# Optimization experiments

Hardware: AMD Instinct MI355X
Metric: run time of the kernel (lower is better)

The kernel has to match this reference:

```python
import jax, jax.numpy as jnp
import numpy as np

DIM = 256
HEADS = 8
WIN = 8
N = WIN * WIN          # 64 tokens per window
NW = 1024              # windows per image (256x256 map, 8x8 windows)
BATCH = 4
B_ = BATCH * NW        # 4096
HEAD_DIM = DIM // HEADS


def _relative_position_index():
    # identical to the torch buffer construction in WindowAttention.__init__
    coords = np.stack(np.meshgrid(np.arange(WIN), np.arange(WIN), indexing='ij'))  # [2,W,W]
    flat = coords.reshape(2, -1)                                # [2, N]
    rel = flat[:, :, None] - flat[:, None, :]                   # [2, N, N]
    rel = rel.transpose(1, 2, 0).copy()                         # [N, N, 2]
    rel[:, :, 0] += WIN - 1
    rel[:, :, 1] += WIN - 1
    rel[:, :, 0] *= 2 * WIN - 1
    return jnp.asarray(rel.sum(-1), dtype=jnp.int32)            # [N, N], values in [0, 225)


def setup_inputs() -> dict:
    key = jax.random.key(0)
    ks = jax.random.split(key, 9)
    std = 0.02
    return {
        'x': jax.random.normal(ks[0], (B_, N, DIM), dtype=jnp.float32),
        'mask': jax.random.normal(ks[1], (NW, N, N), dtype=jnp.float32),
        'w_q': jax.random.normal(ks[2], (DIM, DIM), dtype=jnp.float32) * std,
        'b_q': jnp.zeros((DIM,), dtype=jnp.float32),
        'w_kv': jax.random.normal(ks[3], (2 * DIM, DIM), dtype=jnp.float32) * std,
        'b_kv': jnp.zeros((2 * DIM,), dtype=jnp.float32),
        'bias_table': jax.random.normal(ks[4], ((2 * WIN - 1) ** 2, HEADS), dtype=jnp.float32) * std,
        'w_o': jax.random.normal(ks[5], (DIM, DIM), dtype=jnp.float32) * std,
        'b_o': jnp.zeros((DIM,), dtype=jnp.float32),
        'rp_index': _relative_position_index(),
    }


def reference(x, mask, w_q, b_q, w_kv, b_kv, bias_table, w_o, b_o, rp_index):
    Bw, n, c = x.shape
    h, d = HEADS, c // HEADS
    scale = d ** -0.5

    # linear QKV projection (LinearProjection with attn_kv=None)
    q = (x @ w_q.T + b_q).reshape(Bw, n, h, d).transpose(0, 2, 1, 3)      # [B_, H, N, D]
    kv = (x @ w_kv.T + b_kv).reshape(Bw, n, 2, h, d).transpose(2, 0, 3, 1, 4)
    k, v = kv[0], kv[1]                                                    # [B_, H, N, D]

    # scaled QK^T
    attn = jnp.einsum('bhnd,bhmd->bhnm', q * scale, k)                     # [B_, H, N, N]

    # gathered relative position bias (ratio = 1 since attn_kv is None)
    bias = bias_table[rp_index]                                            # [N, N, H]
    attn = attn + bias.transpose(2, 0, 1)[None]                            # broadcast over B_

    # per-window additive mask
    nW = mask.shape[0]
    attn = attn.reshape(Bw // nW, nW, h, n, n) + mask[None, :, None]
    attn = attn.reshape(Bw, h, n, n)

    attn = jax.nn.softmax(attn, axis=-1)

    out = jnp.einsum('bhnm,bhmd->bhnd', attn, v)                           # [B_, H, N, D]
    out = out.transpose(0, 2, 1, 3).reshape(Bw, n, c)
    return out @ w_o.T + b_o
```

## Files before the change

kernel.cpp:

```cpp
#include <hip/hip_runtime.h>
#include <hip/hip_bf16.h>
#include <stdint.h>

typedef __bf16 bf16_t;
typedef bf16_t bf16x8 __attribute__((ext_vector_type(8)));
typedef bf16_t bf16x4 __attribute__((ext_vector_type(4)));
typedef bf16_t bf16x2 __attribute__((ext_vector_type(2)));
typedef float f32x4 __attribute__((ext_vector_type(4)));
typedef uint32_t u32x4 __attribute__((ext_vector_type(4)));

#define WS_WKV_OFF 65536
#define WS_WO_OFF  196608
#define WS_B8_OFF  524288
#define QSCALE 0.17677669529663687f

__global__ __launch_bounds__(256) void prep_kernel(
    const float* __restrict__ wq, const float* __restrict__ wkv,
    const float* __restrict__ wo, const float* __restrict__ bt,
    const int* __restrict__ rp,
    bf16_t* __restrict__ wsq, bf16_t* __restrict__ wskv,
    bf16_t* __restrict__ wso, float* __restrict__ bias8) {
  int t = blockIdx.x * 256 + threadIdx.x;
  if (t < 65536)  wsq[t]  = (bf16_t)(wq[t] * QSCALE);
  if (t < 131072) wskv[t] = (bf16_t)wkv[t];
  if (t < 65536)  wso[t]  = (bf16_t)wo[t];
  if (t < 4096) {
    int idx = rp[t];
#pragma unroll
    for (int h = 0; h < 8; ++h) bias8[h * 4096 + t] = bt[idx * 8 + h];
  }
}

__device__ __forceinline__ bf16x8 xpose_frag(uint32_t e0, uint32_t e1,
                                             uint32_t o0, uint32_t o1,
                                             int ad0, int ad1, bool hi) {
  uint32_t v0e = (uint32_t)__builtin_amdgcn_ds_bpermute(ad0, (int)e0);
  uint32_t v0o = (uint32_t)__builtin_amdgcn_ds_bpermute(ad0, (int)o0);
  uint32_t v1e = (uint32_t)__builtin_amdgcn_ds_bpermute(ad0, (int)e1);
  uint32_t v1o = (uint32_t)__builtin_amdgcn_ds_bpermute(ad0, (int)o1);
  uint32_t v2e = (uint32_t)__builtin_amdgcn_ds_bpermute(ad1, (int)e0);
  uint32_t v2o = (uint32_t)__builtin_amdgcn_ds_bpermute(ad1, (int)o0);
  uint32_t v3e = (uint32_t)__builtin_amdgcn_ds_bpermute(ad1, (int)e1);
  uint32_t v3o = (uint32_t)__builtin_amdgcn_ds_bpermute(ad1, (int)o1);
  u32x4 r;
  r.x = hi ? v0o : v0e;
  r.y = hi ? v1o : v1e;
  r.z = hi ? v2o : v2e;
  r.w = hi ? v3o : v3e;
  return __builtin_bit_cast(bf16x8, r);
}

__device__ __forceinline__ uint32_t pk2(float a, float b) {
  bf16x2 t = {(bf16_t)a, (bf16_t)b};
  return __builtin_bit_cast(uint32_t, t);
}

__global__ __launch_bounds__(512, 4) void win_attn_kernel(
    const float* __restrict__ x, const float* __restrict__ mask,
    const float* __restrict__ bq, const float* __restrict__ bkv,
    const float* __restrict__ bo,
    const bf16_t* __restrict__ wsq, const bf16_t* __restrict__ wskv,
    const bf16_t* __restrict__ wso, const float* __restrict__ bias8,
    float* __restrict__ out) {
  __shared__ bf16_t lds[35328];
  const int b    = blockIdx.x;
  const int tid  = threadIdx.x;
  const int h    = tid >> 6;
  const int lane = tid & 63;
  const int lrow = lane & 15;
  const int lgrp = lane >> 4;
  const bool hi  = (lgrp & 2) != 0;
  const int ad0  = ((((2 * lgrp) & 3) << 4) + lrow) << 2;
  const int ad1  = ((((2 * lgrp + 1) & 3) << 4) + lrow) << 2;
  const f32x4 zf = {0.f, 0.f, 0.f, 0.f};

  {
    const float4* xv = (const float4*)(x + (size_t)b * 16384);
#pragma unroll
    for (int j = 0; j < 8; ++j) {
      int i4 = j * 512 + tid;
      float4 v = xv[i4];
      int e = i4 * 4;
      int r = e >> 8, c = e & 255;
      bf16x4 w = {(bf16_t)v.x, (bf16_t)v.y, (bf16_t)v.z, (bf16_t)v.w};
      *(bf16x4*)(lds + r * 264 + c) = w;
    }
  }
  __syncthreads();

  bf16_t* ldsVt = lds + 16896 + h * 2304;

  {
    const bf16_t* WVh = wskv + (256 + h * 32) * 256;
    float bv0 = bkv[256 + h * 32 + lrow];
    float bv1 = bkv[256 + h * 32 + 16 + lrow];
#pragma unroll
    for (int vh = 0; vh < 2; ++vh) {
      f32x4 av[2][2];
      av[0][0] = av[0][1] = av[1][0] = av[1][1] = zf;
#pragma unroll
      for (int ks = 0; ks < 8; ++ks) {
        bf16x8 xa[2];
#pragma unroll
        for (int i = 0; i < 2; ++i)
          xa[i] = *(const bf16x8*)(lds + ((vh * 2 + i) * 16 + lrow) * 264 + ks * 32 + lgrp * 8);
        bf16x8 wvf[2];
#pragma unroll
        for (int tn = 0; tn < 2; ++tn)
          wvf[tn] = *(const bf16x8*)(WVh + (tn * 16 + lrow) * 256 + ks * 32 + lgrp * 8);
#pragma unroll
        for (int i = 0; i < 2; ++i)
#pragma unroll
          for (int tn = 0; tn < 2; ++tn)
            av[i][tn] = __builtin_amdgcn_mfma_f32_16x16x32_bf16(xa[i], wvf[tn], av[i][tn], 0, 0, 0);
      }
#pragma unroll
      for (int i = 0; i < 2; ++i)
#pragma unroll
        for (int tn = 0; tn < 2; ++tn) {
          float bv = tn ? bv1 : bv0;
          bf16x4 vv;
#pragma unroll
          for (int r = 0; r < 4; ++r) vv[r] = (bf16_t)(av[i][tn][r] + bv);
          *(bf16x4*)(ldsVt + (tn * 16 + lrow) * 72 + (vh * 2 + i) * 16 + lgrp * 4) = vv;
        }
    }
  }

  bf16x8 qb[4], ka[4];
  {
    const bf16_t* WQh = wsq + h * 32 * 256;
#pragma unroll
    for (int qh = 0; qh < 2; ++qh) {
      f32x4 aq[2][2];
      aq[0][0] = aq[0][1] = aq[1][0] = aq[1][1] = zf;
#pragma unroll
      for (int ks = 0; ks < 8; ++ks) {
        bf16x8 xb[2];
#pragma unroll
        for (int i = 0; i < 2; ++i)
          xb[i] = *(const bf16x8*)(lds + ((qh * 2 + i) * 16 + lrow) * 264 + ks * 32 + lgrp * 8);
        bf16x8 wqf[2];
#pragma unroll
        for (int tm = 0; tm < 2; ++tm)
          wqf[tm] = *(const bf16x8*)(WQh + (tm * 16 + lrow) * 256 + ks * 32 + lgrp * 8);
#pragma unroll
        for (int tm = 0; tm < 2; ++tm)
#pragma unroll
          for (int i = 0; i < 2; ++i)
            aq[tm][i] = __builtin_amdgcn_mfma_f32_16x16x32_bf16(wqf[tm], xb[i], aq[tm][i], 0, 0, 0);
      }
      uint32_t pq[2][2][2];
#pragma unroll
      for (int tm = 0; tm < 2; ++tm) {
        float4 b4 = *(const float4*)(bq + h * 32 + tm * 16 + lgrp * 4);
#pragma unroll
        for (int i = 0; i < 2; ++i) {
          pq[tm][i][0] = pk2(aq[tm][i][0] + b4.x * QSCALE, aq[tm][i][1] + b4.y * QSCALE);
          pq[tm][i][1] = pk2(aq[tm][i][2] + b4.z * QSCALE, aq[tm][i][3] + b4.w * QSCALE);
        }
      }
#pragma unroll
      for (int i = 0; i < 2; ++i)
        qb[qh * 2 + i] = xpose_frag(pq[0][i][0], pq[0][i][1], pq[1][i][0], pq[1][i][1], ad0, ad1, hi);
    }
  }
  {
    const bf16_t* WKh = wskv + h * 32 * 256;
#pragma unroll
    for (int kh = 0; kh < 2; ++kh) {
      f32x4 ak2[2][2];
      ak2[0][0] = ak2[0][1] = ak2[1][0] = ak2[1][1] = zf;
#pragma unroll
      for (int ks = 0; ks < 8; ++ks) {
        bf16x8 xb[2];
#pragma unroll
        for (int i = 0; i < 2; ++i)
          xb[i] = *(const bf16x8*)(lds + ((kh * 2 + i) * 16 + lrow) * 264 + ks * 32 + lgrp * 8);
        bf16x8 wkf[2];
#pragma unroll
        for (int tm = 0; tm < 2; ++tm)
          wkf[tm] = *(const bf16x8*)(WKh + (tm * 16 + lrow) * 256 + ks * 32 + lgrp * 8);
#pragma unroll
        for (int tm = 0; tm < 2; ++tm)
#pragma unroll
          for (int i = 0; i < 2; ++i)
            ak2[tm][i] = __builtin_amdgcn_mfma_f32_16x16x32_bf16(wkf[tm], xb[i], ak2[tm][i], 0, 0, 0);
      }
      uint32_t pk[2][2][2];
#pragma unroll
      for (int tm = 0; tm < 2; ++tm) {
        float4 k4 = *(const float4*)(bkv + h * 32 + tm * 16 + lgrp * 4);
#pragma unroll
        for (int i = 0; i < 2; ++i) {
          pk[tm][i][0] = pk2(ak2[tm][i][0] + k4.x, ak2[tm][i][1] + k4.y);
          pk[tm][i][1] = pk2(ak2[tm][i][2] + k4.z, ak2[tm][i][3] + k4.w);
        }
      }
#pragma unroll
      for (int i = 0; i < 2; ++i)
        ka[kh * 2 + i] = xpose_frag(pk[0][i][0], pk[0][i][1], pk[1][i][0], pk[1][i][1], ad0, ad1, hi);
    }
  }

  __syncthreads();

  const float* maskw = mask + (size_t)(b & 1023) * 4096;
  const float* biash = bias8 + h * 4096;
#pragma unroll
  for (int qt = 0; qt < 4; ++qt) {
    f32x4 st[4];
#pragma unroll
    for (int tm = 0; tm < 4; ++tm)
      st[tm] = __builtin_amdgcn_mfma_f32_16x16x32_bf16(ka[tm], qb[qt], zf, 0, 0, 0);
    int q = qt * 16 + lrow;
    float sm = 0.f;
#pragma unroll
    for (int tm = 0; tm < 4; ++tm) {
      int kb = tm * 16 + lgrp * 4;
      float4 mb = *(const float4*)(maskw + q * 64 + kb);
      float4 bb = *(const float4*)(biash + q * 64 + kb);
#pragma unroll
      for (int r = 0; r < 4; ++r) {
        float madd = (r == 0) ? (mb.x + bb.x) : (r == 1) ? (mb.y + bb.y)
                   : (r == 2) ? (mb.z + bb.z) : (mb.w + bb.w);
        float p = __expf(st[tm][r] + madd);
        st[tm][r] = p;
        sm += p;
      }
    }
    sm += __shfl_xor(sm, 16);
    sm += __shfl_xor(sm, 32);
    float rs = 1.0f / sm;
    uint32_t ppk[4][2];
#pragma unroll
    for (int tm = 0; tm < 4; ++tm) {
      ppk[tm][0] = pk2(st[tm][0] * rs, st[tm][1] * rs);
      ppk[tm][1] = pk2(st[tm][2] * rs, st[tm][3] * rs);
    }
    bf16x8 paf[2];
#pragma unroll
    for (int kf = 0; kf < 2; ++kf)
      paf[kf] = xpose_frag(ppk[2 * kf][0], ppk[2 * kf][1],
                           ppk[2 * kf + 1][0], ppk[2 * kf + 1][1], ad0, ad1, hi);
    f32x4 o[2] = {zf, zf};
#pragma unroll
    for (int dt = 0; dt < 2; ++dt)
#pragma unroll
      for (int kf = 0; kf < 2; ++kf) {
        bf16x8 vf = *(const bf16x8*)(ldsVt + (dt * 16 + lrow) * 72 + kf * 32 + lgrp * 8);
        o[dt] = __builtin_amdgcn_mfma_f32_16x16x32_bf16(paf[kf], vf, o[dt], 0, 0, 0);
      }
#pragma unroll
    for (int dt = 0; dt < 2; ++dt)
#pragma unroll
      for (int r = 0; r < 4; ++r)
        lds[(qt * 16 + lgrp * 4 + r) * 264 + h * 32 + dt * 16 + lrow] = (bf16_t)o[dt][r];
  }
  __syncthreads();

  const int nb = h * 32;
  float* outw = out + (size_t)b * 16384;
#pragma unroll
  for (int half = 0; half < 2; ++half) {
    f32x4 oc[2][2];
#pragma unroll
    for (int tm = 0; tm < 2; ++tm)
#pragma unroll
      for (int tn = 0; tn < 2; ++tn) oc[tm][tn] = zf;
#pragma unroll
    for (int ks = 0; ks < 8; ++ks) {
      bf16x8 ao[2];
#pragma unroll
      for (int tm = 0; tm < 2; ++tm)
        ao[tm] = *(const bf16x8*)(lds + ((half * 2 + tm) * 16 + lrow) * 264 + ks * 32 + lgrp * 8);
      bf16x8 bw[2];
#pragma unroll
      for (int tn = 0; tn < 2; ++tn)
        bw[tn] = *(const bf16x8*)(wso + (nb + tn * 16 + lrow) * 256 + ks * 32 + lgrp * 8);
#pragma unroll
      for (int tm = 0; tm < 2; ++tm)
#pragma unroll
        for (int tn = 0; tn < 2; ++tn)
          oc[tm][tn] = __builtin_amdgcn_mfma_f32_16x16x32_bf16(ao[tm], bw[tn], oc[tm][tn], 0, 0, 0);
    }
#pragma unroll
    for (int tn = 0; tn < 2; ++tn) {
      float bov = bo[nb + tn * 16 + lrow];
#pragma unroll
      for (int tm = 0; tm < 2; ++tm)
#pragma unroll
        for (int r = 0; r < 4; ++r)
          outw[((half * 2 + tm) * 16 + lgrp * 4 + r) * 256 + nb + tn * 16 + lrow] =
              oc[tm][tn][r] + bov;
    }
  }
}

extern "C" void kernel_launch(void* const* d_in, const int* in_sizes, int n_in,
                              void* d_out, int out_size, void* d_ws, size_t ws_size,
                              hipStream_t stream) {
  const float* x    = (const float*)d_in[0];
  const float* mask = (const float*)d_in[1];
  const float* wq   = (const float*)d_in[2];
  const float* bq   = (const float*)d_in[3];
  const float* wkv  = (const float*)d_in[4];
  const float* bkv  = (const float*)d_in[5];
  const float* bt   = (const float*)d_in[6];
  const float* wo   = (const float*)d_in[7];
  const float* bo   = (const float*)d_in[8];
  const int*   rp   = (const int*)d_in[9];
  float* out = (float*)d_out;

  bf16_t* wsq  = (bf16_t*)d_ws;
  bf16_t* wskv = wsq + WS_WKV_OFF;
  bf16_t* wso  = wsq + WS_WO_OFF;
  float*  bias8 = (float*)((char*)d_ws + WS_B8_OFF);

  prep_kernel<<<512, 256, 0, stream>>>(wq, wkv, wo, bt, rp, wsq, wskv, wso, bias8);

  win_attn_kernel<<<4096, 512, 0, stream>>>(
      x, mask, bq, bkv, bo, wsq, wskv, wso, bias8, out);
}
```

Before: 568.5 us.

## Process two windows per block and prefetch next window's x via global_load_lds

```diff
diff --git a/kernel.cpp b/kernel.cpp
--- a/kernel.cpp
+++ b/kernel.cpp
@@ -55,15 +55,21 @@
   return __builtin_bit_cast(uint32_t, t);
 }
 
-__global__ __launch_bounds__(512, 4) void win_attn_kernel(
+typedef const __attribute__((address_space(1))) void gas_void;
+typedef __attribute__((address_space(3))) void las_void;
+
+#define LDS_TOTAL_BYTES 136192
+
+__global__ __launch_bounds__(512, 2) void win_attn_kernel(
     const float* __restrict__ x, const float* __restrict__ mask,
     const float* __restrict__ bq, const float* __restrict__ bkv,
     const float* __restrict__ bo,
     const bf16_t* __restrict__ wsq, const bf16_t* __restrict__ wskv,
     const bf16_t* __restrict__ wso, const float* __restrict__ bias8,
     float* __restrict__ out) {
-  __shared__ bf16_t lds[35328];
-  const int b    = blockIdx.x;
+  extern __shared__ bf16_t lds[];
+  float* xraw = (float*)(lds + 35328);
+  const int blk  = blockIdx.x;
   const int tid  = threadIdx.x;
   const int h    = tid >> 6;
   const int lane = tid & 63;
@@ -73,227 +79,252 @@
   const int ad0  = ((((2 * lgrp) & 3) << 4) + lrow) << 2;
   const int ad1  = ((((2 * lgrp + 1) & 3) << 4) + lrow) << 2;
   const f32x4 zf = {0.f, 0.f, 0.f, 0.f};
+  bf16_t* ldsVt = lds + 16896 + h * 2304;
 
   {
-    const float4* xv = (const float4*)(x + (size_t)b * 16384);
+    const float* xsrc = x + (size_t)(2 * blk) * 16384;
 #pragma unroll
     for (int j = 0; j < 8; ++j) {
-      int i4 = j * 512 + tid;
-      float4 v = xv[i4];
-      int e = i4 * 4;
-      int r = e >> 8, c = e & 255;
-      bf16x4 w = {(bf16_t)v.x, (bf16_t)v.y, (bf16_t)v.z, (bf16_t)v.w};
-      *(bf16x4*)(lds + r * 264 + c) = w;
+      int off = h * 2048 + j * 256;
+      __builtin_amdgcn_global_load_lds((gas_void*)(xsrc + off + lane * 4),
+                                       (las_void*)(xraw + off), 16, 0, 0);
     }
   }
   __syncthreads();
 
-  bf16_t* ldsVt = lds + 16896 + h * 2304;
-
-  {
-    const bf16_t* WVh = wskv + (256 + h * 32) * 256;
-    float bv0 = bkv[256 + h * 32 + lrow];
-    float bv1 = bkv[256 + h * 32 + 16 + lrow];
-#pragma unroll
-    for (int vh = 0; vh < 2; ++vh) {
-      f32x4 av[2][2];
-      av[0][0] = av[0][1] = av[1][0] = av[1][1] = zf;
+#pragma unroll 1
+  for (int w = 0; w < 2; ++w) {
+    const int b = 2 * blk + w;
+
+    {
+#pragma unroll
+      for (int j = 0; j < 8; ++j) {
+        int i4 = j * 512 + tid;
+        float4 v = *(const float4*)(xraw + i4 * 4);
+        int e = i4 * 4;
+        int r = e >> 8, c = e & 255;
+        bf16x4 wv = {(bf16_t)v.x, (bf16_t)v.y, (bf16_t)v.z, (bf16_t)v.w};
+        *(bf16x4*)(lds + r * 264 + c) = wv;
+      }
+    }
+    __syncthreads();
+
+    if (w == 0) {
+      const float* xsrc = x + (size_t)(2 * blk + 1) * 16384;
+#pragma unroll
+      for (int j = 0; j < 8; ++j) {
+        int off = h * 2048 + j * 256;
+        __builtin_amdgcn_global_load_lds((gas_void*)(xsrc + off + lane * 4),
+                                         (las_void*)(xraw + off), 16, 0, 0);
+      }
+    }
+
+    {
+      const bf16_t* WVh = wskv + (256 + h * 32) * 256;
+      float bv0 = bkv[256 + h * 32 + lrow];
+      float bv1 = bkv[256 + h * 32 + 16 + lrow];
+#pragma unroll
+      for (int vh = 0; vh < 2; ++vh) {
+        f32x4 av[2][2];
+        av[0][0] = av[0][1] = av[1][0] = av[1][1] = zf;
+#pragma unroll
+        for (int ks = 0; ks < 8; ++ks) {
+          bf16x8 xa[2];
+#pragma unroll
+          for (int i = 0; i < 2; ++i)
+            xa[i] = *(const bf16x8*)(lds + ((vh * 2 + i) * 16 + lrow) * 264 + ks * 32 + lgrp * 8);
+          bf16x8 wvf[2];
+#pragma unroll
+          for (int tn = 0; tn < 2; ++tn)
+            wvf[tn] = *(const bf16x8*)(WVh + (tn * 16 + lrow) * 256 + ks * 32 + lgrp * 8);
+#pragma unroll
+          for (int i = 0; i < 2; ++i)
+#pragma unroll
+            for (int tn = 0; tn < 2; ++tn)
+              av[i][tn] = __builtin_amdgcn_mfma_f32_16x16x32_bf16(xa[i], wvf[tn], av[i][tn], 0, 0, 0);
+        }
+#pragma unroll
+        for (int i = 0; i < 2; ++i)
+#pragma unroll
+          for (int tn = 0; tn < 2; ++tn) {
+            float bv = tn ? bv1 : bv0;
+            bf16x4 vv;
+#pragma unroll
+            for (int r = 0; r < 4; ++r) vv[r] = (bf16_t)(av[i][tn][r] + bv);
+            *(bf16x4*)(ldsVt + (tn * 16 + lrow) * 72 + (vh * 2 + i) * 16 + lgrp * 4) = vv;
+          }
+      }
+    }
+
+    bf16x8 qb[4], ka[4];
+    {
+      const bf16_t* WQh = wsq + h * 32 * 256;
+#pragma unroll
+      for (int qh = 0; qh < 2; ++qh) {
+        f32x4 aq[2][2];
+        aq[0][0] = aq[0][1] = aq[1][0] = aq[1][1] = zf;
+#pragma unroll
+        for (int ks = 0; ks < 8; ++ks) {
+          bf16x8 xb[2];
+#pragma unroll
+          for (int i = 0; i < 2; ++i)
+            xb[i] = *(const bf16x8*)(lds + ((qh * 2 + i) * 16 + lrow) * 264 + ks * 32 + lgrp * 8);
+          bf16x8 wqf[2];
+#pragma unroll
+          for (int tm = 0; tm < 2; ++tm)
+            wqf[tm] = *(const bf16x8*)(WQh + (tm * 16 + lrow) * 256 + ks * 32 + lgrp * 8);
+#pragma unroll
+          for (int tm = 0; tm < 2; ++tm)
+#pragma unroll
+            for (int i = 0; i < 2; ++i)
+              aq[tm][i] = __builtin_amdgcn_mfma_f32_16x16x32_bf16(wqf[tm], xb[i], aq[tm][i], 0, 0, 0);
+        }
+        uint32_t pq[2][2][2];
+#pragma unroll
+        for (int tm = 0; tm < 2; ++tm) {
+          float4 b4 = *(const float4*)(bq + h * 32 + tm * 16 + lgrp * 4);
+#pragma unroll
+          for (int i = 0; i < 2; ++i) {
+            pq[tm][i][0] = pk2(aq[tm][i][0] + b4.x * QSCALE, aq[tm][i][1] + b4.y * QSCALE);
+            pq[tm][i][1] = pk2(aq[tm][i][2] + b4.z * QSCALE, aq[tm][i][3] + b4.w * QSCALE);
+          }
+        }
+#pragma unroll
+        for (int i = 0; i < 2; ++i)
+          qb[qh * 2 + i] = xpose_frag(pq[0][i][0], pq[0][i][1], pq[1][i][0], pq[1][i][1], ad0, ad1, hi);
+      }
+    }
+    {
+      const bf16_t* WKh = wskv + h * 32 * 256;
+#pragma unroll
+      for (int kh = 0; kh < 2; ++kh) {
+        f32x4 ak2[2][2];
+        ak2[0][0] = ak2[0][1] = ak2[1][0] = ak2[1][1] = zf;
+#pragma unroll
+        for (int ks = 0; ks < 8; ++ks) {
+          bf16x8 xb[2];
+#pragma unroll
+          for (int i = 0; i < 2; ++i)
+            xb[i] = *(const bf16x8*)(lds + ((kh * 2 + i) * 16 + lrow) * 264 + ks * 32 + lgrp * 8);
+          bf16x8 wkf[2];
+#pragma unroll
+          for (int tm = 0; tm < 2; ++tm)
+            wkf[tm] = *(const bf16x8*)(WKh + (tm * 16 + lrow) * 256 + ks * 32 + lgrp * 8);
+#pragma unroll
+          for (int tm = 0; tm < 2; ++tm)
+#pragma unroll
+            for (int i = 0; i < 2; ++i)
+              ak2[tm][i] = __builtin_amdgcn_mfma_f32_16x16x32_bf16(wkf[tm], xb[i], ak2[tm][i], 0, 0, 0);
+        }
+        uint32_t pkk[2][2][2];
+#pragma unroll
+        for (int tm = 0; tm < 2; ++tm) {
+          float4 k4 = *(const float4*)(bkv + h * 32 + tm * 16 + lgrp * 4);
+#pragma unroll
+          for (int i = 0; i < 2; ++i) {
+            pkk[tm][i][0] = pk2(ak2[tm][i][0] + k4.x, ak2[tm][i][1] + k4.y);
+            pkk[tm][i][1] = pk2(ak2[tm][i][2] + k4.z, ak2[tm][i][3] + k4.w);
+          }
+        }
+#pragma unroll
+        for (int i = 0; i < 2; ++i)
+          ka[kh * 2 + i] = xpose_frag(pkk[0][i][0], pkk[0][i][1], pkk[1][i][0], pkk[1][i][1], ad0, ad1, hi);
+      }
+    }
+
+    __syncthreads();
+
+    const float* maskw = mask + (size_t)(b & 1023) * 4096;
+    const float* biash = bias8 + h * 4096;
+#pragma unroll
+    for (int qt = 0; qt < 4; ++qt) {
+      f32x4 st[4];
+#pragma unroll
+      for (int tm = 0; tm < 4; ++tm)
+        st[tm] = __builtin_amdgcn_mfma_f32_16x16x32_bf16(ka[tm], qb[qt], zf, 0, 0, 0);
+      int q = qt * 16 + lrow;
+      float sm = 0.f;
+#pragma unroll
+      for (int tm = 0; tm < 4; ++tm) {
+        int kb = tm * 16 + lgrp * 4;
+        float4 mb = *(const float4*)(maskw + q * 64 + kb);
+        float4 bb = *(const float4*)(biash + q * 64 + kb);
+#pragma unroll
+        for (int r = 0; r < 4; ++r) {
+          float madd = (r == 0) ? (mb.x + bb.x) : (r == 1) ? (mb.y + bb.y)
+                     : (r == 2) ? (mb.z + bb.z) : (mb.w + bb.w);
+          float p = __expf(st[tm][r] + madd);
+          st[tm][r] = p;
+          sm += p;
+        }
+      }
+      sm += __shfl_xor(sm, 16);
+      sm += __shfl_xor(sm, 32);
+      float rs = 1.0f / sm;
+      uint32_t ppk[4][2];
+#pragma unroll
+      for (int tm = 0; tm < 4; ++tm) {
+        ppk[tm][0] = pk2(st[tm][0] * rs, st[tm][1] * rs);
+        ppk[tm][1] = pk2(st[tm][2] * rs, st[tm][3] * rs);
+      }
+      bf16x8 paf[2];
+#pragma unroll
+      for (int kf = 0; kf < 2; ++kf)
+        paf[kf] = xpose_frag(ppk[2 * kf][0], ppk[2 * kf][1],
+                             ppk[2 * kf + 1][0], ppk[2 * kf + 1][1], ad0, ad1, hi);
+      f32x4 o[2] = {zf, zf};
+#pragma unroll
+      for (int dt = 0; dt < 2; ++dt)
+#pragma unroll
+        for (int kf = 0; kf < 2; ++kf) {
+          bf16x8 vf = *(const bf16x8*)(ldsVt + (dt * 16 + lrow) * 72 + kf * 32 + lgrp * 8);
+          o[dt] = __builtin_amdgcn_mfma_f32_16x16x32_bf16(paf[kf], vf, o[dt], 0, 0, 0);
+        }
+#pragma unroll
+      for (int dt = 0; dt < 2; ++dt)
+#pragma unroll
+        for (int r = 0; r < 4; ++r)
+          lds[(qt * 16 + lgrp * 4 + r) * 264 + h * 32 + dt * 16 + lrow] = (bf16_t)o[dt][r];
+    }
+    __syncthreads();
+
+    const int nb = h * 32;
+    float* outw = out + (size_t)b * 16384;
+#pragma unroll
+    for (int half = 0; half < 2; ++half) {
+      f32x4 oc[2][2];
+#pragma unroll
+      for (int tm = 0; tm < 2; ++tm)
+#pragma unroll
+        for (int tn = 0; tn < 2; ++tn) oc[tm][tn] = zf;
 #pragma unroll
       for (int ks = 0; ks < 8; ++ks) {
-        bf16x8 xa[2];
-#pragma unroll
-        for (int i = 0; i < 2; ++i)
-          xa[i] = *(const bf16x8*)(lds + ((vh * 2 + i) * 16 + lrow) * 264 + ks * 32 + lgrp * 8);
-        bf16x8 wvf[2];
+        bf16x8 ao[2];
+#pragma unroll
+        for (int tm = 0; tm < 2; ++tm)
+          ao[tm] = *(const bf16x8*)(lds + ((half * 2 + tm) * 16 + lrow) * 264 + ks * 32 + lgrp * 8);
+        bf16x8 bw[2];
 #pragma unroll
         for (int tn = 0; tn < 2; ++tn)
-          wvf[tn] = *(const bf16x8*)(WVh + (tn * 16 + lrow) * 256 + ks * 32 + lgrp * 8);
-#pragma unroll
-        for (int i = 0; i < 2; ++i)
+          bw[tn] = *(const bf16x8*)(wso + (nb + tn * 16 + lrow) * 256 + ks * 32 + lgrp * 8);
+#pragma unroll
+        for (int tm = 0; tm < 2; ++tm)
 #pragma unroll
           for (int tn = 0; tn < 2; ++tn)
-            av[i][tn] = __builtin_amdgcn_mfma_f32_16x16x32_bf16(xa[i], wvf[tn], av[i][tn], 0, 0, 0);
-      }
-#pragma unroll
-      for (int i = 0; i < 2; ++i)
-#pragma unroll
-        for (int tn = 0; tn < 2; ++tn) {
-          float bv = tn ? bv1 : bv0;
-          bf16x4 vv;
-#pragma unroll
-          for (int r = 0; r < 4; ++r) vv[r] = (bf16_t)(av[i][tn][r] + bv);
-          *(bf16x4*)(ldsVt + (tn * 16 + lrow) * 72 + (vh * 2 + i) * 16 + lgrp * 4) = vv;
-        }
-    }
-  }
-
-  bf16x8 qb[4], ka[4];
-  {
-    const bf16_t* WQh = wsq + h * 32 * 256;
-#pragma unroll
-    for (int qh = 0; qh < 2; ++qh) {
-      f32x4 aq[2][2];
-      aq[0][0] = aq[0][1] = aq[1][0] = aq[1][1] = zf;
-#pragma unroll
-      for (int ks = 0; ks < 8; ++ks) {
-        bf16x8 xb[2];
-#pragma unroll
-        for (int i = 0; i < 2; ++i)
-          xb[i] = *(const bf16x8*)(lds + ((qh * 2 + i) * 16 + lrow) * 264 + ks * 32 + lgrp * 8);
-        bf16x8 wqf[2];
+            oc[tm][tn] = __builtin_amdgcn_mfma_f32_16x16x32_bf16(ao[tm], bw[tn], oc[tm][tn], 0, 0, 0);
+      }
+#pragma unroll
+      for (int tn = 0; tn < 2; ++tn) {
+        float bov = bo[nb + tn * 16 + lrow];
 #pragma unroll
         for (int tm = 0; tm < 2; ++tm)
-          wqf[tm] = *(const bf16x8*)(WQh + (tm * 16 + lrow) * 256 + ks * 32 + lgrp * 8);
-#pragma unroll
-        for (int tm = 0; tm < 2; ++tm)
-#pragma unroll
-          for (int i = 0; i < 2; ++i)
-            aq[tm][i] = __builtin_amdgcn_mfma_f32_16x16x32_bf16(wqf[tm], xb[i], aq[tm][i], 0, 0, 0);
-      }
-      uint32_t pq[2][2][2];
-#pragma unroll
-      for (int tm = 0; tm < 2; ++tm) {
-        float4 b4 = *(const float4*)(bq + h * 32 + tm * 16 + lgrp * 4);
-#pragma unroll
-        for (int i = 0; i < 2; ++i) {
-          pq[tm][i][0] = pk2(aq[tm][i][0] + b4.x * QSCALE, aq[tm][i][1] + b4.y * QSCALE);
-          pq[tm][i][1] = pk2(aq[tm][i][2] + b4.z * QSCALE, aq[tm][i][3] + b4.w * QSCALE);
-        }
-      }
-#pragma unroll
-      for (int i = 0; i < 2; ++i)
-        qb[qh * 2 + i] = xpose_frag(pq[0][i][0], pq[0][i][1], pq[1][i][0], pq[1][i][1], ad0, ad1, hi);
-    }
-  }
-  {
-    const bf16_t* WKh = wskv + h * 32 * 256;
-#pragma unroll
-    for (int kh = 0; kh < 2; ++kh) {
-      f32x4 ak2[2][2];
-      ak2[0][0] = ak2[0][1] = ak2[1][0] = ak2[1][1] = zf;
-#pragma unroll
-      for (int ks = 0; ks < 8; ++ks) {
-        bf16x8 xb[2];
-#pragma unroll
-        for (int i = 0; i < 2; ++i)
-          xb[i] = *(const bf16x8*)(lds + ((kh * 2 + i) * 16 + lrow) * 264 + ks * 32 + lgrp * 8);
-        bf16x8 wkf[2];
-#pragma unroll
-        for (int tm = 0; tm < 2; ++tm)
-          wkf[tm] = *(const bf16x8*)(WKh + (tm * 16 + lrow) * 256 + ks * 32 + lgrp * 8);
-#pragma unroll
-        for (int tm = 0; tm < 2; ++tm)
-#pragma unroll
-          for (int i = 0; i < 2; ++i)
-            ak2[tm][i] = __builtin_amdgcn_mfma_f32_16x16x32_bf16(wkf[tm], xb[i], ak2[tm][i], 0, 0, 0);
-      }
-      uint32_t pk[2][2][2];
-#pragma unroll
-      for (int tm = 0; tm < 2; ++tm) {
-        float4 k4 = *(const float4*)(bkv + h * 32 + tm * 16 + lgrp * 4);
-#pragma unroll
-        for (int i = 0; i < 2; ++i) {
-          pk[tm][i][0] = pk2(ak2[tm][i][0] + k4.x, ak2[tm][i][1] + k4.y);
-          pk[tm][i][1] = pk2(ak2[tm][i][2] + k4.z, ak2[tm][i][3] + k4.w);
-        }
-      }
-#pragma unroll
-      for (int i = 0; i < 2; ++i)
-        ka[kh * 2 + i] = xpose_frag(pk[0][i][0], pk[0][i][1], pk[1][i][0], pk[1][i][1], ad0, ad1, hi);
-    }
-  }
-
-  __syncthreads();
-
-  const float* maskw = mask + (size_t)(b & 1023) * 4096;
-  const float* biash = bias8 + h * 4096;
-#pragma unroll
-  for (int qt = 0; qt < 4; ++qt) {
-    f32x4 st[4];
-#pragma unroll
-    for (int tm = 0; tm < 4; ++tm)
-      st[tm] = __builtin_amdgcn_mfma_f32_16x16x32_bf16(ka[tm], qb[qt], zf, 0, 0, 0);
-    int q = qt * 16 + lrow;
-    float sm = 0.f;
-#pragma unroll
-    for (int tm = 0; tm < 4; ++tm) {
-      int kb = tm * 16 + lgrp * 4;
-      float4 mb = *(const float4*)(maskw + q * 64 + kb);
-      float4 bb = *(const float4*)(biash + q * 64 + kb);
-#pragma unroll
-      for (int r = 0; r < 4; ++r) {
-        float madd = (r == 0) ? (mb.x + bb.x) : (r == 1) ? (mb.y + bb.y)
-                   : (r == 2) ? (mb.z + bb.z) : (mb.w + bb.w);
-        float p = __expf(st[tm][r] + madd);
-        st[tm][r] = p;
-        sm += p;
-      }
-    }
-    sm += __shfl_xor(sm, 16);
-    sm += __shfl_xor(sm, 32);
-    float rs = 1.0f / sm;
-    uint32_t ppk[4][2];
-#pragma unroll
-    for (int tm = 0; tm < 4; ++tm) {
-      ppk[tm][0] = pk2(st[tm][0] * rs, st[tm][1] * rs);
-      ppk[tm][1] = pk2(st[tm][2] * rs, st[tm][3] * rs);
-    }
-    bf16x8 paf[2];
-#pragma unroll
-    for (int kf = 0; kf < 2; ++kf)
-      paf[kf] = xpose_frag(ppk[2 * kf][0], ppk[2 * kf][1],
-                           ppk[2 * kf + 1][0], ppk[2 * kf + 1][1], ad0, ad1, hi);
-    f32x4 o[2] = {zf, zf};
-#pragma unroll
-    for (int dt = 0; dt < 2; ++dt)
-#pragma unroll
-      for (int kf = 0; kf < 2; ++kf) {
-        bf16x8 vf = *(const bf16x8*)(ldsVt + (dt * 16 + lrow) * 72 + kf * 32 + lgrp * 8);
-        o[dt] = __builtin_amdgcn_mfma_f32_16x16x32_bf16(paf[kf], vf, o[dt], 0, 0, 0);
-      }
-#pragma unroll
-    for (int dt = 0; dt < 2; ++dt)
-#pragma unroll
-      for (int r = 0; r < 4; ++r)
-        lds[(qt * 16 + lgrp * 4 + r) * 264 + h * 32 + dt * 16 + lrow] = (bf16_t)o[dt][r];
-  }
-  __syncthreads();
-
-  const int nb = h * 32;
-  float* outw = out + (size_t)b * 16384;
-#pragma unroll
-  for (int half = 0; half < 2; ++half) {
-    f32x4 oc[2][2];
-#pragma unroll
-    for (int tm = 0; tm < 2; ++tm)
-#pragma unroll
-      for (int tn = 0; tn < 2; ++tn) oc[tm][tn] = zf;
-#pragma unroll
-    for (int ks = 0; ks < 8; ++ks) {
-      bf16x8 ao[2];
-#pragma unroll
-      for (int tm = 0; tm < 2; ++tm)
-        ao[tm] = *(const bf16x8*)(lds + ((half * 2 + tm) * 16 + lrow) * 264 + ks * 32 + lgrp * 8);
-      bf16x8 bw[2];
-#pragma unroll
-      for (int tn = 0; tn < 2; ++tn)
-        bw[tn] = *(const bf16x8*)(wso + (nb + tn * 16 + lrow) * 256 + ks * 32 + lgrp * 8);
-#pragma unroll
-      for (int tm = 0; tm < 2; ++tm)
-#pragma unroll
-        for (int tn = 0; tn < 2; ++tn)
-          oc[tm][tn] = __builtin_amdgcn_mfma_f32_16x16x32_bf16(ao[tm], bw[tn], oc[tm][tn], 0, 0, 0);
-    }
-#pragma unroll
-    for (int tn = 0; tn < 2; ++tn) {
-      float bov = bo[nb + tn * 16 + lrow];
-#pragma unroll
-      for (int tm = 0; tm < 2; ++tm)
-#pragma unroll
-        for (int r = 0; r < 4; ++r)
-          outw[((half * 2 + tm) * 16 + lgrp * 4 + r) * 256 + nb + tn * 16 + lrow] =
-              oc[tm][tn][r] + bov;
-    }
+#pragma unroll
+          for (int r = 0; r < 4; ++r)
+            outw[((half * 2 + tm) * 16 + lgrp * 4 + r) * 256 + nb + tn * 16 + lrow] =
+                oc[tm][tn][r] + bov;
+      }
+    }
+    __syncthreads();
   }
 }
 
@@ -319,6 +350,8 @@
 
   prep_kernel<<<512, 256, 0, stream>>>(wq, wkv, wo, bt, rp, wsq, wskv, wso, bias8);
 
-  win_attn_kernel<<<4096, 512, 0, stream>>>(
+  (void)hipFuncSetAttribute((const void*)win_attn_kernel,
+                            hipFuncAttributeMaxDynamicSharedMemorySize, LDS_TOTAL_BYTES);
+  win_attn_kernel<<<2048, 512, LDS_TOTAL_BYTES, stream>>>(
       x, mask, bq, bkv, bo, wsq, wskv, wso, bias8, out);
 }
```

After: 1.526 ms. 168% more time.
